# Kernel tuning notes

Measured on AMD Instinct MI355X. Metric: run time of the kernel, lower is better.

Reference implementation:

```python
import jax, jax.numpy as jnp
import numpy as np

T, D, H, E, A = 4096, 1024, 2048, 8, 2


def setup_inputs() -> dict:
    key = jax.random.key(0)
    k1, k2, k3, k4, k5 = jax.random.split(key, 5)
    x = jax.random.normal(k1, (T, D), dtype=jnp.float32)
    expert_indices = jax.random.randint(k2, (T, A), 0, E, dtype=jnp.int64)
    scale = 0.02  # keep activations numerically sane (torch.randn init is unscaled)
    w_gate = jax.random.normal(k3, (E, H, D), dtype=jnp.float32) * scale
    w_up = jax.random.normal(k4, (E, H, D), dtype=jnp.float32) * scale
    w_down = jax.random.normal(k5, (E, D, H), dtype=jnp.float32) * scale
    return {"x": x, "expert_indices": expert_indices,
            "w_gate": w_gate, "w_up": w_up, "w_down": w_down}


def reference(x, expert_indices, w_gate, w_up, w_down):
    # Math identical to: gather per-token expert weights then einsum, but
    # computed as dense all-expert GEMMs + small activation gathers so we
    # never materialize the (T, A, H, D) gathered weight tensors.
    zg = jnp.einsum('td,ehd->teh', x, w_gate)   # (T, E, H)
    zu = jnp.einsum('td,ehd->teh', x, w_up)     # (T, E, H)
    idx = expert_indices[:, :, None]            # (T, A, 1)
    g = jnp.take_along_axis(zg, idx, axis=1)    # (T, A, H)
    u = jnp.take_along_axis(zu, idx, axis=1)    # (T, A, H)
    h = jax.nn.silu(g) * u                      # (T, A, H)
    # Down projection: route h back to its expert with one-hot, dense GEMM.
    oh = jax.nn.one_hot(expert_indices, E, dtype=h.dtype)  # (T, A, E)
    he = jnp.einsum('tah,tae->taeh', h, oh)     # (T, A, E, H)
    out = jnp.einsum('taeh,edh->tad', he, w_down)  # (T, A, D)
    return out
```

## Files before the change

kernel.cpp:

```cpp
#include <hip/hip_runtime.h>

#define NE 8
#define TA 8192
#define MAXT 40
#define MAXPAD (MAXT*256)

typedef __attribute__((ext_vector_type(4)))  float f32x4;
typedef __attribute__((ext_vector_type(16))) float f32x16;
typedef __attribute__((ext_vector_type(8)))  short s16x8;

#define WS_CUR  8
#define WS_META 16
#define WS_TEXP 18
#define WS_PERM 256

#define WAITVM(N) asm volatile("s_waitcnt vmcnt(" #N ")" ::: "memory")
#define LGKM0()   asm volatile("s_waitcnt lgkmcnt(0)" ::: "memory")
#define BAR()     asm volatile("s_barrier" ::: "memory")

__device__ __forceinline__ unsigned short f2bf(float f) {
  unsigned u = __builtin_bit_cast(unsigned, f);
  u += 0x7FFFu + ((u >> 16) & 1u);
  return (unsigned short)(u >> 16);
}

__device__ __forceinline__ void glds16(const unsigned short* g, unsigned short* l) {
  __builtin_amdgcn_global_load_lds(
      (const __attribute__((address_space(1))) unsigned int*)g,
      (__attribute__((address_space(3))) unsigned int*)l, 16, 0, 0);
}

__global__ void k_route(const int* __restrict__ idx, int* __restrict__ ws) {
  __shared__ int cnt[NE];
  int t = threadIdx.x;
  if (t < NE) cnt[t] = 0;
  __syncthreads();
  int e0[8];
#pragma unroll
  for (int k = 0; k < 8; ++k) { e0[k] = idx[t + k * 1024]; atomicAdd(&cnt[e0[k]], 1); }
  __syncthreads();
  if (t == 0) {
    int off = 0, ti = 0;
    for (int e = 0; e < NE; ++e) {
      ws[WS_CUR + e] = off;
      int c = cnt[e];
      int ntl = (c + 255) >> 8;
      for (int k = 0; k < ntl; ++k) ws[WS_TEXP + ti++] = e;
      off += ntl << 8;
    }
    ws[WS_META] = ti;
    ws[WS_META + 1] = off;
  }
#pragma unroll
  for (int k = 0; k < MAXPAD / 1024; ++k) ws[WS_PERM + t + k * 1024] = -1;
  __syncthreads();
#pragma unroll
  for (int k = 0; k < 8; ++k) {
    int p = atomicAdd(&ws[WS_CUR + e0[k]], 1);
    ws[WS_PERM + p] = t + k * 1024;
  }
}

__global__ void k_cvt_gu2(const float* __restrict__ g, const float* __restrict__ u,
                          unsigned short* __restrict__ d) {
  int t = blockIdx.x * 256 + threadIdx.x;
  int i = t * 8;
  int dd = i & 1023;
  int h = (i >> 10) & 2047;
  int e = i >> 21;
  int dr = (e << 12) + ((h >> 5) << 6) + (h & 31);
  f32x4 a = *(const f32x4*)(g + i);
  f32x4 b = *(const f32x4*)(g + i + 4);
  s16x8 o;
  o[0] = (short)f2bf(a[0]); o[1] = (short)f2bf(a[1]);
  o[2] = (short)f2bf(a[2]); o[3] = (short)f2bf(a[3]);
  o[4] = (short)f2bf(b[0]); o[5] = (short)f2bf(b[1]);
  o[6] = (short)f2bf(b[2]); o[7] = (short)f2bf(b[3]);
  *(s16x8*)(d + (size_t)dr * 1024 + dd) = o;
  a = *(const f32x4*)(u + i);
  b = *(const f32x4*)(u + i + 4);
  o[0] = (short)f2bf(a[0]); o[1] = (short)f2bf(a[1]);
  o[2] = (short)f2bf(a[2]); o[3] = (short)f2bf(a[3]);
  o[4] = (short)f2bf(b[0]); o[5] = (short)f2bf(b[1]);
  o[6] = (short)f2bf(b[2]); o[7] = (short)f2bf(b[3]);
  *(s16x8*)(d + (size_t)(dr + 32) * 1024 + dd) = o;
}

__global__ void k_cvt(const float* __restrict__ s, unsigned short* __restrict__ d) {
  int i = (blockIdx.x * 256 + threadIdx.x) * 8;
  f32x4 a = *(const f32x4*)(s + i);
  f32x4 b = *(const f32x4*)(s + i + 4);
  s16x8 o;
  o[0] = (short)f2bf(a[0]); o[1] = (short)f2bf(a[1]);
  o[2] = (short)f2bf(a[2]); o[3] = (short)f2bf(a[3]);
  o[4] = (short)f2bf(b[0]); o[5] = (short)f2bf(b[1]);
  o[6] = (short)f2bf(b[2]); o[7] = (short)f2bf(b[3]);
  *(s16x8*)(d + i) = o;
}

__global__ void k_gather(const float* __restrict__ x, const int* __restrict__ ws,
                         unsigned short* __restrict__ xb) {
  int tid = blockIdx.x * 256 + threadIdx.x;
  int r = tid >> 7;
  int c = (tid & 127) << 3;
  int ta = ws[WS_PERM + r];
  s16x8 o = {0,0,0,0,0,0,0,0};
  if (ta >= 0) {
    const float* xp = x + (size_t)(ta >> 1) * 1024 + c;
    f32x4 a = *(const f32x4*)xp;
    f32x4 b = *(const f32x4*)(xp + 4);
    o[0] = (short)f2bf(a[0]); o[1] = (short)f2bf(a[1]);
    o[2] = (short)f2bf(a[2]); o[3] = (short)f2bf(a[3]);
    o[4] = (short)f2bf(b[0]); o[5] = (short)f2bf(b[1]);
    o[6] = (short)f2bf(b[2]); o[7] = (short)f2bf(b[3]);
  }
  *(s16x8*)(xb + (size_t)r * 1024 + c) = o;
}


#define STG(BUF, KSH, KO)                                              \
  {                                                                    \
    unsigned short* ld = &L[BUF][(KSH) * 4096 + tid * 8];              \
    glds16(gA + (KO), ld);                                             \
    glds16(gB + (KO), ld + 8192);                                      \
  }

#define PHASE(BUF, KSH, KON, ACC0, ACC1)                               \
  {                                                                    \
    WAITVM(2);                                                         \
    BAR();                                                             \
    STG((BUF) ^ 1, KSH, KON);                                          \
    const unsigned short* Lb = &L[BUF][(KSH) * 4096];                  \
    s16x8 a0 = *(const s16x8*)&Lb[aoff + sca0];                        \
    s16x8 a1 = *(const s16x8*)&Lb[aoff + sca1];                        \
    s16x8 b00 = *(const s16x8*)&Lb[boff + scb0];                       \
    s16x8 b01 = *(const s16x8*)&Lb[boff + 1024 + scb0];                \
    s16x8 b10 = *(const s16x8*)&Lb[boff + scb1];                       \
    s16x8 b11 = *(const s16x8*)&Lb[boff + 1024 + scb1];                \
    __builtin_amdgcn_s_setprio(1);                                     \
    ACC0 = __builtin_amdgcn_mfma_f32_32x32x16_bf16(a0, b00, ACC0, 0, 0, 0); \
    ACC1 = __builtin_amdgcn_mfma_f32_32x32x16_bf16(a0, b01, ACC1, 0, 0, 0); \
    ACC0 = __builtin_amdgcn_mfma_f32_32x32x16_bf16(a1, b10, ACC0, 0, 0, 0); \
    ACC1 = __builtin_amdgcn_mfma_f32_32x32x16_bf16(a1, b11, ACC1, 0, 0, 0); \
    __builtin_amdgcn_s_setprio(0);                                     \
    LGKM0();                                                           \
    BAR();                                                             \
  }

#define GEOM_COMMON                                                    \
  int tid = threadIdx.x, lane = tid & 63, wid = tid >> 6;              \
  int wm = wid >> 1, wn = wid & 1;                                     \
  int r31 = lane & 31, kg = lane >> 5;                                 \
  int sr = tid >> 2, sp = tid & 3;                                     \
  int ss = sp ^ ((sr >> 1) & 3);                                       \
  int ra = wm * 32 + r31;                                              \
  int rb = wn * 64 + r31;                                              \
  int swa = (ra >> 1) & 3, swb = (rb >> 1) & 3;                        \
  int aoff = ra * 32;                                                  \
  int boff = 8192 + rb * 32;                                           \
  int sca0 = ((kg ^ swa)) << 3, sca1 = (((2 | kg) ^ swa)) << 3;        \
  int scb0 = ((kg ^ swb)) << 3, scb1 = (((2 | kg) ^ swb)) << 3;

__global__ __launch_bounds__(512, 4) void k_gemm1(
    const unsigned short* __restrict__ xb, const unsigned short* __restrict__ wgu,
    unsigned short* __restrict__ hb, const int* __restrict__ ws) {
  int mt = blockIdx.y;
  if (mt >= ws[WS_META] * 2) return;
  int e = ws[WS_TEXP + (mt >> 1)];
  int nt = blockIdx.x;

  __shared__ unsigned short L[2][16384];

  GEOM_COMMON

  const unsigned short* gA = xb  + (size_t)(mt * 128 + sr) * 1024 + ss * 8;
  const unsigned short* gB = wgu + (size_t)(e * 4096 + nt * 128 + sr) * 1024 + ss * 8;

  f32x16 accg = {}, accu = {};

  STG(0, 0, 0)
  STG(0, 1, 32)

#pragma unroll 2
  for (int t = 0; t < 16; ++t) {
    int tn = (t + 1 < 16 ? t + 1 : t) * 64;
    PHASE(t & 1, 0, tn,      accg, accu)
    PHASE(t & 1, 1, tn + 32, accg, accu)
  }

  int hrow0 = mt * 128 + wm * 32;
  int hcol  = (nt * 2 + wn) * 32 + r31;
#pragma unroll
  for (int r = 0; r < 16; ++r) {
    int crow = (r & 3) + 8 * (r >> 2) + 4 * kg;
    float g = accg[r];
    float u = accu[r];
    float h = (g / (1.f + __expf(-g))) * u;
    hb[(size_t)(hrow0 + crow) * 2048 + hcol] = f2bf(h);
  }
}

__global__ __launch_bounds__(512, 4) void k_gemm2(
    const unsigned short* __restrict__ hb, const unsigned short* __restrict__ wdb,
    float* __restrict__ out, const int* __restrict__ ws) {
  int mt = blockIdx.y;
  if (mt >= ws[WS_META] * 2) return;
  int e = ws[WS_TEXP + (mt >> 1)];
  int nt = blockIdx.x;

  __shared__ unsigned short L[2][16384];

  GEOM_COMMON

  const unsigned short* gA = hb  + (size_t)(mt * 128 + sr) * 2048 + ss * 8;
  const unsigned short* gB = wdb + (size_t)(e * 1024 + nt * 128 + sr) * 2048 + ss * 8;

  f32x16 acc0 = {}, acc1 = {};

  STG(0, 0, 0)
  STG(0, 1, 32)

#pragma unroll 2
  for (int t = 0; t < 32; ++t) {
    int tn = (t + 1 < 32 ? t + 1 : t) * 64;
    PHASE(t & 1, 0, tn,      acc0, acc1)
    PHASE(t & 1, 1, tn + 32, acc0, acc1)
  }

  int prow0 = mt * 128 + wm * 32;
  int dcol  = nt * 128 + wn * 64 + r31;
#pragma unroll
  for (int r = 0; r < 16; ++r) {
    int crow = (r & 3) + 8 * (r >> 2) + 4 * kg;
    int ta = ws[WS_PERM + prow0 + crow];
    if (ta >= 0) {
      out[(size_t)ta * 1024 + dcol]      = acc0[r];
      out[(size_t)ta * 1024 + dcol + 32] = acc1[r];
    }
  }
}

extern "C" void kernel_launch(void* const* d_in, const int* in_sizes, int n_in,
                              void* d_out, int out_size, void* d_ws, size_t ws_size,
                              hipStream_t stream) {
  const float* x   = (const float*)d_in[0];
  const int*   idx = (const int*)d_in[1];
  const float* wg  = (const float*)d_in[2];
  const float* wu  = (const float*)d_in[3];
  const float* wd  = (const float*)d_in[4];
  float* out = (float*)d_out;

  int*  wsi = (int*)d_ws;
  char* wsb = (char*)d_ws;
  const size_t OFF_XB  = 65536;
  const size_t OFF_WDB = 65536;
  const size_t OFF_WGU = 65536 + (size_t)NE * 1024 * 2048 * 2;
  const size_t OFF_HB  = OFF_WGU + (size_t)NE * 4096 * 1024 * 2;
  unsigned short* xbuf = (unsigned short*)(wsb + OFF_XB);
  unsigned short* wdb  = (unsigned short*)(wsb + OFF_WDB);
  unsigned short* wgu  = (unsigned short*)(wsb + OFF_WGU);
  unsigned short* hb   = (unsigned short*)(wsb + OFF_HB);

  k_route<<<1, 1024, 0, stream>>>(idx, wsi);
  k_cvt_gu2<<<(NE * 2048 * 1024) / (256 * 8), 256, 0, stream>>>(wg, wu, wgu);
  k_gather<<<(MAXPAD * 128) / 256, 256, 0, stream>>>(x, wsi, xbuf);

  k_gemm1<<<dim3(32, MAXT * 2), 512, 0, stream>>>(xbuf, wgu, hb, wsi);

  k_cvt<<<(NE * 1024 * 2048) / (256 * 8), 256, 0, stream>>>(wd, wdb);

  k_gemm2<<<dim3(8, MAXT * 2), 512, 0, stream>>>(hb, wdb, out, wsi);
}
```

Measured before the change: 266.4 us.

## Enlarge GEMM tiles to 256x256 and split-K the down projection with atomics

Both expert GEMMs now use 256x256 block tiles with a 64-deep K step, split into four MFMA sub-phases per K step. Each warp computes a 4x2 grid of 32x32 MFMA tiles, which raises reuse of each LDS fragment and cuts global and LDS traffic per FLOP. The down-projection GEMM splits K into two halves across blocks. Their partial sums are combined with float atomic adds into an output that is zeroed first by a memset. In exchange, the LDS footprint doubles to 128KB per block, occupancy drops, the pipeline now waits for all outstanding loads each iteration, and the atomic accumulation makes the output order nondeterministic.

After: 315.3 us. 1.18x slower.

```diff
diff --git a/kernel.cpp b/kernel.cpp
--- a/kernel.cpp
+++ b/kernel.cpp
@@ -15,7 +15,6 @@
 #define WS_PERM 256
 
 #define WAITVM(N) asm volatile("s_waitcnt vmcnt(" #N ")" ::: "memory")
-#define LGKM0()   asm volatile("s_waitcnt lgkmcnt(0)" ::: "memory")
 #define BAR()     asm volatile("s_barrier" ::: "memory")
 
 __device__ __forceinline__ unsigned short f2bf(float f) {
@@ -118,126 +117,143 @@
 }
 
 
-#define STG(BUF, KSH, KO)                                              \
+#define STG4(GPTR, LDST, KO, RSTRIDE)                                  \
+  _Pragma("unroll")                                                    \
+  for (int j = 0; j < 4; ++j)                                          \
+    glds16((GPTR) + (size_t)j * 64 * (RSTRIDE) + (KO), (LDST) + j * 4096 + tid * 8);
+
+#define PHASE(LC, KS, ACCX, ACCY, BO1)                                 \
   {                                                                    \
-    unsigned short* ld = &L[BUF][(KSH) * 4096 + tid * 8];              \
-    glds16(gA + (KO), ld);                                             \
-    glds16(gB + (KO), ld + 8192);                                      \
-  }
-
-#define PHASE(BUF, KSH, KON, ACC0, ACC1)                               \
-  {                                                                    \
-    WAITVM(2);                                                         \
-    BAR();                                                             \
-    STG((BUF) ^ 1, KSH, KON);                                          \
-    const unsigned short* Lb = &L[BUF][(KSH) * 4096];                  \
-    s16x8 a0 = *(const s16x8*)&Lb[aoff + sca0];                        \
-    s16x8 a1 = *(const s16x8*)&Lb[aoff + sca1];                        \
-    s16x8 b00 = *(const s16x8*)&Lb[boff + scb0];                       \
-    s16x8 b01 = *(const s16x8*)&Lb[boff + 1024 + scb0];                \
-    s16x8 b10 = *(const s16x8*)&Lb[boff + scb1];                       \
-    s16x8 b11 = *(const s16x8*)&Lb[boff + 1024 + scb1];                \
+    int sc = (((KS) * 2 + kg) ^ x7) << 3;                              \
+    s16x8 a0 = *(const s16x8*)&(LC)[aof + sc];                         \
+    s16x8 a1 = *(const s16x8*)&(LC)[aof + 2048 + sc];                  \
+    s16x8 a2 = *(const s16x8*)&(LC)[aof + 4096 + sc];                  \
+    s16x8 a3 = *(const s16x8*)&(LC)[aof + 6144 + sc];                  \
+    s16x8 bx = *(const s16x8*)&(LC)[bgo + sc];                         \
+    s16x8 by = *(const s16x8*)&(LC)[bgo + (BO1) + sc];                 \
     __builtin_amdgcn_s_setprio(1);                                     \
-    ACC0 = __builtin_amdgcn_mfma_f32_32x32x16_bf16(a0, b00, ACC0, 0, 0, 0); \
-    ACC1 = __builtin_amdgcn_mfma_f32_32x32x16_bf16(a0, b01, ACC1, 0, 0, 0); \
-    ACC0 = __builtin_amdgcn_mfma_f32_32x32x16_bf16(a1, b10, ACC0, 0, 0, 0); \
-    ACC1 = __builtin_amdgcn_mfma_f32_32x32x16_bf16(a1, b11, ACC1, 0, 0, 0); \
+    ACCX[0] = __builtin_amdgcn_mfma_f32_32x32x16_bf16(a0, bx, ACCX[0], 0, 0, 0); \
+    ACCY[0] = __builtin_amdgcn_mfma_f32_32x32x16_bf16(a0, by, ACCY[0], 0, 0, 0); \
+    ACCX[1] = __builtin_amdgcn_mfma_f32_32x32x16_bf16(a1, bx, ACCX[1], 0, 0, 0); \
+    ACCY[1] = __builtin_amdgcn_mfma_f32_32x32x16_bf16(a1, by, ACCY[1], 0, 0, 0); \
+    ACCX[2] = __builtin_amdgcn_mfma_f32_32x32x16_bf16(a2, bx, ACCX[2], 0, 0, 0); \
+    ACCY[2] = __builtin_amdgcn_mfma_f32_32x32x16_bf16(a2, by, ACCY[2], 0, 0, 0); \
+    ACCX[3] = __builtin_amdgcn_mfma_f32_32x32x16_bf16(a3, bx, ACCX[3], 0, 0, 0); \
+    ACCY[3] = __builtin_amdgcn_mfma_f32_32x32x16_bf16(a3, by, ACCY[3], 0, 0, 0); \
     __builtin_amdgcn_s_setprio(0);                                     \
-    LGKM0();                                                           \
-    BAR();                                                             \
-  }
-
-#define GEOM_COMMON                                                    \
+  }
+
+#define GEOM                                                           \
   int tid = threadIdx.x, lane = tid & 63, wid = tid >> 6;              \
-  int wm = wid >> 1, wn = wid & 1;                                     \
-  int r31 = lane & 31, kg = lane >> 5;                                 \
-  int sr = tid >> 2, sp = tid & 3;                                     \
-  int ss = sp ^ ((sr >> 1) & 3);                                       \
-  int ra = wm * 32 + r31;                                              \
-  int rb = wn * 64 + r31;                                              \
-  int swa = (ra >> 1) & 3, swb = (rb >> 1) & 3;                        \
-  int aoff = ra * 32;                                                  \
-  int boff = 8192 + rb * 32;                                           \
-  int sca0 = ((kg ^ swa)) << 3, sca1 = (((2 | kg) ^ swa)) << 3;        \
-  int scb0 = ((kg ^ swb)) << 3, scb1 = (((2 | kg) ^ swb)) << 3;
-
-__global__ __launch_bounds__(512, 4) void k_gemm1(
+  int wm = wid >> 2, wn = wid & 3;                                     \
+  int r31 = lane & 31, kg = lane >> 5, x7 = r31 & 7;                   \
+  int srow = tid >> 3;                                                 \
+  int cs = (tid & 7) ^ (srow & 7);                                     \
+  int aof = (wm * 128 + r31) * 64;                                     \
+  int bgo = 16384 + (wn * 64 + r31) * 64;
+
+__global__ __launch_bounds__(512) void k_gemm1(
     const unsigned short* __restrict__ xb, const unsigned short* __restrict__ wgu,
     unsigned short* __restrict__ hb, const int* __restrict__ ws) {
   int mt = blockIdx.y;
-  if (mt >= ws[WS_META] * 2) return;
-  int e = ws[WS_TEXP + (mt >> 1)];
+  if (mt >= ws[WS_META]) return;
+  int e = ws[WS_TEXP + mt];
   int nt = blockIdx.x;
 
-  __shared__ unsigned short L[2][16384];
-
-  GEOM_COMMON
-
-  const unsigned short* gA = xb  + (size_t)(mt * 128 + sr) * 1024 + ss * 8;
-  const unsigned short* gB = wgu + (size_t)(e * 4096 + nt * 128 + sr) * 1024 + ss * 8;
-
-  f32x16 accg = {}, accu = {};
-
-  STG(0, 0, 0)
-  STG(0, 1, 32)
-
-#pragma unroll 2
+  __shared__ unsigned short L[2][32768];
+
+  GEOM
+
+  const unsigned short* gA = xb  + (size_t)(mt * 256 + srow) * 1024 + cs * 8;
+  const unsigned short* gB = wgu + (size_t)(e * 4096 + nt * 256 + srow) * 1024 + cs * 8;
+
+  f32x16 accg[4] = {}, accu[4] = {};
+
+  STG4(gA, &L[0][0],     0, 1024)
+  STG4(gB, &L[0][16384], 0, 1024)
+
   for (int t = 0; t < 16; ++t) {
-    int tn = (t + 1 < 16 ? t + 1 : t) * 64;
-    PHASE(t & 1, 0, tn,      accg, accu)
-    PHASE(t & 1, 1, tn + 32, accg, accu)
-  }
-
-  int hrow0 = mt * 128 + wm * 32;
-  int hcol  = (nt * 2 + wn) * 32 + r31;
-#pragma unroll
-  for (int r = 0; r < 16; ++r) {
-    int crow = (r & 3) + 8 * (r >> 2) + 4 * kg;
-    float g = accg[r];
-    float u = accu[r];
-    float h = (g / (1.f + __expf(-g))) * u;
-    hb[(size_t)(hrow0 + crow) * 2048 + hcol] = f2bf(h);
-  }
-}
-
-__global__ __launch_bounds__(512, 4) void k_gemm2(
+    const unsigned short* Lc = &L[t & 1][0];
+    unsigned short* Ln = &L[(t & 1) ^ 1][0];
+    int ko = (t + 1) * 64;
+    WAITVM(0);
+    BAR();
+    if (t < 15) { STG4(gA, Ln, ko, 1024) }
+    PHASE(Lc, 0, accg, accu, 2048)
+    BAR();
+    if (t < 15) { STG4(gB, Ln + 16384, ko, 1024) }
+    PHASE(Lc, 1, accg, accu, 2048)
+    BAR();
+    PHASE(Lc, 2, accg, accu, 2048)
+    BAR();
+    PHASE(Lc, 3, accg, accu, 2048)
+  }
+
+  int hrow0 = mt * 256 + wm * 128;
+  int hcol  = nt * 128 + wn * 32 + r31;
+#pragma unroll
+  for (int mi = 0; mi < 4; ++mi)
+#pragma unroll
+    for (int r = 0; r < 16; ++r) {
+      int crow = (r & 3) + 8 * (r >> 2) + 4 * kg;
+      float g = accg[mi][r];
+      float u = accu[mi][r];
+      float h = (g / (1.f + __expf(-g))) * u;
+      hb[(size_t)(hrow0 + mi * 32 + crow) * 2048 + hcol] = f2bf(h);
+    }
+}
+
+__global__ __launch_bounds__(512) void k_gemm2(
     const unsigned short* __restrict__ hb, const unsigned short* __restrict__ wdb,
     float* __restrict__ out, const int* __restrict__ ws) {
   int mt = blockIdx.y;
-  if (mt >= ws[WS_META] * 2) return;
-  int e = ws[WS_TEXP + (mt >> 1)];
-  int nt = blockIdx.x;
-
-  __shared__ unsigned short L[2][16384];
-
-  GEOM_COMMON
-
-  const unsigned short* gA = hb  + (size_t)(mt * 128 + sr) * 2048 + ss * 8;
-  const unsigned short* gB = wdb + (size_t)(e * 1024 + nt * 128 + sr) * 2048 + ss * 8;
-
-  f32x16 acc0 = {}, acc1 = {};
-
-  STG(0, 0, 0)
-  STG(0, 1, 32)
-
-#pragma unroll 2
-  for (int t = 0; t < 32; ++t) {
-    int tn = (t + 1 < 32 ? t + 1 : t) * 64;
-    PHASE(t & 1, 0, tn,      acc0, acc1)
-    PHASE(t & 1, 1, tn + 32, acc0, acc1)
-  }
-
-  int prow0 = mt * 128 + wm * 32;
-  int dcol  = nt * 128 + wn * 64 + r31;
-#pragma unroll
-  for (int r = 0; r < 16; ++r) {
-    int crow = (r & 3) + 8 * (r >> 2) + 4 * kg;
-    int ta = ws[WS_PERM + prow0 + crow];
-    if (ta >= 0) {
-      out[(size_t)ta * 1024 + dcol]      = acc0[r];
-      out[(size_t)ta * 1024 + dcol + 32] = acc1[r];
+  if (mt >= ws[WS_META]) return;
+  int e = ws[WS_TEXP + mt];
+  int nt = blockIdx.x & 3;
+  int kb = (blockIdx.x >> 2) * 1024;
+
+  __shared__ unsigned short L[2][32768];
+
+  GEOM
+
+  const unsigned short* gA = hb  + (size_t)(mt * 256 + srow) * 2048 + kb + cs * 8;
+  const unsigned short* gB = wdb + (size_t)(e * 1024 + nt * 256 + srow) * 2048 + kb + cs * 8;
+
+  f32x16 acc0[4] = {}, acc1[4] = {};
+
+  STG4(gA, &L[0][0],     0, 2048)
+  STG4(gB, &L[0][16384], 0, 2048)
+
+  for (int t = 0; t < 16; ++t) {
+    const unsigned short* Lc = &L[t & 1][0];
+    unsigned short* Ln = &L[(t & 1) ^ 1][0];
+    int ko = (t + 1) * 64;
+    WAITVM(0);
+    BAR();
+    if (t < 15) { STG4(gA, Ln, ko, 2048) }
+    PHASE(Lc, 0, acc0, acc1, 2048)
+    BAR();
+    if (t < 15) { STG4(gB, Ln + 16384, ko, 2048) }
+    PHASE(Lc, 1, acc0, acc1, 2048)
+    BAR();
+    PHASE(Lc, 2, acc0, acc1, 2048)
+    BAR();
+    PHASE(Lc, 3, acc0, acc1, 2048)
+  }
+
+  int prow0 = mt * 256 + wm * 128;
+  int dcol  = nt * 256 + wn * 64 + r31;
+#pragma unroll
+  for (int mi = 0; mi < 4; ++mi)
+#pragma unroll
+    for (int r = 0; r < 16; ++r) {
+      int crow = (r & 3) + 8 * (r >> 2) + 4 * kg;
+      int ta = ws[WS_PERM + prow0 + mi * 32 + crow];
+      if (ta >= 0) {
+        unsafeAtomicAdd(&out[(size_t)ta * 1024 + dcol],      acc0[mi][r]);
+        unsafeAtomicAdd(&out[(size_t)ta * 1024 + dcol + 32], acc1[mi][r]);
+      }
     }
-  }
 }
 
 extern "C" void kernel_launch(void* const* d_in, const int* in_sizes, int n_in,
@@ -265,9 +281,10 @@
   k_cvt_gu2<<<(NE * 2048 * 1024) / (256 * 8), 256, 0, stream>>>(wg, wu, wgu);
   k_gather<<<(MAXPAD * 128) / 256, 256, 0, stream>>>(x, wsi, xbuf);
 
-  k_gemm1<<<dim3(32, MAXT * 2), 512, 0, stream>>>(xbuf, wgu, hb, wsi);
+  k_gemm1<<<dim3(16, MAXT), 512, 0, stream>>>(xbuf, wgu, hb, wsi);
 
   k_cvt<<<(NE * 1024 * 2048) / (256 * 8), 256, 0, stream>>>(wd, wdb);
 
-  k_gemm2<<<dim3(8, MAXT * 2), 512, 0, stream>>>(hb, wdb, out, wsi);
-}
+  hipMemsetAsync(out, 0, (size_t)out_size * sizeof(float), stream);
+  k_gemm2<<<dim3(8, MAXT), 512, 0, stream>>>(hb, wdb, out, wsi);
+}
```
